# Kernel tuning notes

Measured on AMD Instinct MI355X. Metric: run time of the kernel, lower is better.

## Reference

```python
import jax, jax.numpy as jnp
import numpy as np

N = 1026; DX = 4096; DG = 4096; H0 = 4096; H1 = 2048; H2 = 1024
OUTS = 512; NL = 10; JH = 2048; E = 32832; K = 128; ALPHA = 0.05
INS = DX + DG  # 8192, edgeconv1 / joint_gemb input width

def _w(k, fan_in, shape):
    s = 1.0 / np.sqrt(fan_in)
    return jax.random.uniform(k, shape, minval=-s, maxval=s, dtype=jnp.float32)

def setup_inputs() -> dict:
    key = jax.random.key(0)
    ks = jax.random.split(key, 32)
    return dict(
        x=jax.random.normal(ks[0], (N, DX), jnp.float32),
        gx=jax.random.normal(ks[1], (N, DG), jnp.float32),
        edge_index=jax.random.randint(ks[2], (2, E), 0, N, dtype=jnp.int32),
        jw1=_w(ks[3], INS, (INS, JH)), jb1=_w(ks[4], INS, (JH,)),
        jw2=_w(ks[5], JH, (JH, N)), jb2=_w(ks[6], JH, (N,)),
        ec1_w=_w(ks[7], INS, (INS, H0)), ec1_b=_w(ks[8], INS, (H0,)),
        dr_w=_w(ks[9], H0, (H0, H2)), dr_b=_w(ks[10], H0, (H2,)),
        g1_w=_w(ks[11], H0, (H0, H1)), g1_b=_w(ks[12], H0, (H1,)),
        g2_w=_w(ks[13], H1, (H1, H2)), g2_b=_w(ks[14], H1, (H2,)),
        ec2_w=_w(ks[15], H2 + H1 + H0, (H2 + H1 + H0, H2)), ec2_b=_w(ks[16], H2 + H1 + H0, (H2,)),
        ec3_w=_w(ks[17], H2, (H2, OUTS)), ec3_b=_w(ks[18], H2, (OUTS,)),
        out_w=_w(ks[19], OUTS, (OUTS, NL)), out_b=_w(ks[20], OUTS, (NL,)),
    )

def _gdc(A):
    # GDC: self_loop_weight=1, sym norm in, exact PPR (alpha), topk(k, dim=0) sparsify, col norm out
    n = A.shape[0]
    eye = jnp.eye(n, dtype=A.dtype)
    A = A + eye  # self loops, weight 1
    deg = A.sum(axis=1)
    dinv = jax.lax.rsqrt(jnp.where(deg > 0, deg, 1.0))
    T = dinv[:, None] * A * dinv[None, :]          # D^-1/2 (A+I) D^-1/2
    S = ALPHA * jnp.linalg.inv(eye - (1.0 - ALPHA) * T)  # exact PPR diffusion
    vals, idx = jax.lax.top_k(S.T, K)              # top-K per column (dim=0)
    St = jnp.zeros((n, n), S.dtype).at[jnp.arange(n)[:, None], idx].set(vals)
    S = St.T
    csum = S.sum(axis=0)
    return S / jnp.where(csum == 0, 1.0, csum)[None, :]  # col normalization out

def _gcn(h_in, W, b, row, col, n):
    # PyG GCNConv: add self loops, sym-normalized aggregation, then bias
    h = h_in @ W
    deg = jax.ops.segment_sum(jnp.ones(row.shape[0], h.dtype), col, num_segments=n) + 1.0
    dinv = jax.lax.rsqrt(deg)
    agg = jax.ops.segment_sum(h[row] * (dinv[row] * dinv[col])[:, None], col, num_segments=n)
    return agg + h * (dinv * dinv)[:, None] + b

def _forward(x, gx, edge_index, jw1, jb1, jw2, jb2, ec1_w, ec1_b, dr_w, dr_b,
             g1_w, g1_b, g2_w, g2_b, ec2_w, ec2_b, ec3_w, ec3_b, out_w, out_b):
    row, col = edge_index[0], edge_index[1]
    xg = jnp.concatenate([x, gx], axis=1)                    # [N, INS]
    zz = jax.nn.relu(jax.nn.relu(xg @ jw1 + jb1) @ jw2 + jb2)  # joint_gemb -> [N, N] adjacency
    zz = _gdc(zz)
    xn = zz @ x                                              # nconv: dense neighbor aggregation
    z = jax.nn.relu(jnp.concatenate([xn, gx], axis=1) @ ec1_w + ec1_b)  # [N, H0]
    z0 = z @ dr_w + dr_b                                     # [N, H2]
    z1 = jax.nn.relu(_gcn(z + gx, g1_w, g1_b, row, col, N))  # [N, H1]
    z2 = jax.nn.relu(_gcn(z1, g2_w, g2_b, row, col, N))      # [N, H2]
    zc = jax.nn.relu(jnp.concatenate([z, z1, z2], axis=1) @ ec2_w + ec2_b)
    zf = jax.nn.relu((zc + z0) @ ec3_w + ec3_b)
    return zf @ out_w + out_b                                # [N, NL]

def reference(x, gx, edge_index, jw1, jb1, jw2, jb2, ec1_w, ec1_b, dr_w, dr_b,
              g1_w, g1_b, g2_w, g2_b, ec2_w, ec2_b, ec3_w, ec3_b, out_w, out_b):
    return _forward(x, gx, edge_index, jw1, jb1, jw2, jb2, ec1_w, ec1_b, dr_w, dr_b,
                    g1_w, g1_b, g2_w, g2_b, ec2_w, ec2_b, ec3_w, ec3_b, out_w, out_b)
```

## Files before the change

### kernel.cpp

```cpp
#include <hip/hip_runtime.h>
#include <stdint.h>

static constexpr int N_   = 1026;
static constexpr int DX_  = 4096;
static constexpr int DG_  = 4096;
static constexpr int H0_  = 4096;
static constexpr int H1_  = 2048;
static constexpr int H2_  = 1024;
static constexpr int OUTS_= 512;
static constexpr int NL_  = 10;
static constexpr int JH_  = 2048;
static constexpr int E_   = 32832;
static constexpr int K_   = 128;
static constexpr int INS_ = DX_ + DG_;
static constexpr int CAT2_= H0_ + H1_ + H2_;

static constexpr int MP_   = 1152;
static constexpr int KP1_  = 1056;

typedef _Float16 f16;
typedef __attribute__((ext_vector_type(8))) _Float16 f16x8;
typedef __attribute__((ext_vector_type(4))) _Float16 f16x4;
typedef __attribute__((ext_vector_type(4))) float    f32x4;

#define AS1C(p) ((const __attribute__((address_space(1))) unsigned int*)(p))
#define AS3(p)  ((__attribute__((address_space(3))) unsigned int*)(p))

__device__ __forceinline__ void gload16(const f16* g, f16* s) {
    __builtin_amdgcn_global_load_lds(AS1C(g), AS3(s), 16, 0, 0);
}

template<bool RELU, bool DUAL>
__global__ __launch_bounds__(512, DUAL ? 4 : 8)
void gemm_f16x2(int M, int Nc, int Kt, int chunkSteps,
                const f16* __restrict__ Ah, const f16* __restrict__ Al, int lda,
                const f16* __restrict__ Bh, const f16* __restrict__ Bl, int ldb,
                const float* __restrict__ bias, float alpha,
                const float* __restrict__ D, int ldd, float dscale,
                float* __restrict__ C, int ldc,
                f16* __restrict__ oAh, f16* __restrict__ oAl, int ldoa,
                f16* __restrict__ oBh, f16* __restrict__ oBl, int ldob,
                float* __restrict__ P, int Mp, int Ncp)
{
    __shared__ __align__(16) f16 sm[2][DUAL ? 4 : 2][4096];
    const int tid  = threadIdx.x;
    const int lane = tid & 63, w = tid >> 6;
    const int wr = w >> 1, wc = w & 1;
    const int bm = blockIdx.y * 128, bn = blockIdx.x * 128;
    const int z  = blockIdx.z;

    const int totalSteps = Kt >> 5;
    const int sBeg = z * chunkSteps;
    int nst = totalSteps - sBeg; if (nst > chunkSteps) nst = chunkSteps;

    const int srow  = w * 16 + (tid & 15);
    const int skoff = ((tid >> 4) & 3) * 8;
    const size_t arow = (size_t)(bm + srow) * lda + skoff;
    const size_t brow = (size_t)(bn + srow) * ldb + skoff;
    const int wslot = w * 512;
    const int fr = (lane >> 4) * 128 + (lane & 15) * 8;
    const int iaBase = wr * 1024 + fr;
    const int ibBase = wc * 2048 + fr;
    constexpr int PB = DUAL ? 8192 : 4096;

    f32x4 acc[2][4] = {};

    auto stage = [&](int buf, size_t ka) {
        f16* s0 = (f16*)&sm[buf][0][0];
        gload16(Ah + arow + ka, s0 + wslot);
        if constexpr (DUAL) gload16(Al + arow + ka, s0 + 4096 + wslot);
        gload16(Bh + brow + ka, s0 + PB + wslot);
        if constexpr (DUAL) gload16(Bl + brow + ka, s0 + PB + 4096 + wslot);
    };

    if (nst > 0) {
        const size_t kb = (size_t)sBeg * 32;
        stage(0, kb);
        for (int s = 0; s < nst; ++s) {
            if (s + 1 < nst) {
                stage((s + 1) & 1, kb + (size_t)(s + 1) * 32);
                if constexpr (DUAL)
                    asm volatile("s_waitcnt vmcnt(4)\n\ts_barrier" ::: "memory");
                else
                    asm volatile("s_waitcnt vmcnt(2)\n\ts_barrier" ::: "memory");
            } else {
                asm volatile("s_waitcnt vmcnt(0)\n\ts_barrier" ::: "memory");
            }
            const int b = s & 1;
            f16x8 ah[2], al[2], bh4[4], bl4[4];
            #pragma unroll
            for (int i = 0; i < 2; ++i) {
                ah[i] = *(const f16x8*)&sm[b][0][iaBase + i * 512];
                if constexpr (DUAL) al[i] = *(const f16x8*)&sm[b][1][iaBase + i * 512];
            }
            #pragma unroll
            for (int j = 0; j < 4; ++j) {
                bh4[j] = *(const f16x8*)&sm[b][DUAL ? 2 : 1][ibBase + j * 512];
                if constexpr (DUAL) bl4[j] = *(const f16x8*)&sm[b][3][ibBase + j * 512];
            }
            #pragma unroll
            for (int i = 0; i < 2; ++i)
                #pragma unroll
                for (int j = 0; j < 4; ++j) {
                    acc[i][j] = __builtin_amdgcn_mfma_f32_16x16x32_f16(ah[i], bh4[j], acc[i][j], 0, 0, 0);
                    if constexpr (DUAL) {
                        acc[i][j] = __builtin_amdgcn_mfma_f32_16x16x32_f16(ah[i], bl4[j], acc[i][j], 0, 0, 0);
                        acc[i][j] = __builtin_amdgcn_mfma_f32_16x16x32_f16(al[i], bh4[j], acc[i][j], 0, 0, 0);
                    }
                }
            if (s + 1 < nst) asm volatile("s_barrier" ::: "memory");
        }
    }

    const int er = (lane >> 4) * 4;
    const int ec = lane & 15;
    const int m00 = bm + wr * 32, n00 = bn + wc * 64;

    if (P) {
        float* Pz = P + (size_t)z * Mp * Ncp;
        #pragma unroll
        for (int mi = 0; mi < 2; ++mi)
            #pragma unroll
            for (int nj = 0; nj < 4; ++nj) {
                const int gc = n00 + nj * 16 + ec;
                const int gr = m00 + mi * 16 + er;
                float* p = Pz + (size_t)gr * Ncp + gc;
                f32x4 a = acc[mi][nj];
                #pragma unroll
                for (int r = 0; r < 4; ++r) p[(size_t)r * Ncp] = a[r];
            }
        return;
    }

    #pragma unroll
    for (int mi = 0; mi < 2; ++mi) {
        #pragma unroll
        for (int nj = 0; nj < 4; ++nj) {
            const int gcol = n00 + nj * 16 + ec;
            if (gcol >= Nc) continue;
            const float bv = bias ? bias[gcol] : 0.f;
            f32x4 a = acc[mi][nj];
            #pragma unroll
            for (int r = 0; r < 4; ++r) {
                const int grow = m00 + mi * 16 + er + r;
                if (grow >= M) continue;
                float val = alpha * a[r];
                if (D) val = fmaf(dscale, D[(size_t)grow * ldd + gcol], val);
                val += bv;
                if (RELU) val = fmaxf(val, 0.f);
                if (C) C[(size_t)grow * ldc + gcol] = val;
                if (oAh) {
                    f16 h = (f16)val, l = (f16)(val - (float)h);
                    oAh[(size_t)grow * ldoa + gcol] = h;
                    oAl[(size_t)grow * ldoa + gcol] = l;
                }
                if (oBh) {
                    f16 h = (f16)val, l = (f16)(val - (float)h);
                    oBh[(size_t)gcol * ldob + grow] = h;
                    oBl[(size_t)gcol * ldob + grow] = l;
                }
            }
        }
    }
}

template<bool RELU>
__global__ __launch_bounds__(256)
void combine_k(int M, int Nc, int nz, int Mp, int Ncp,
               const float* __restrict__ P,
               const float* __restrict__ bias, float alpha,
               const float* __restrict__ D, int ldd, float dscale,
               float* __restrict__ C, int ldc,
               f16* __restrict__ oAh, f16* __restrict__ oAl, int ldoa,
               f16* __restrict__ oBh, f16* __restrict__ oBl, int ldob)
{
    unsigned idx = blockIdx.x * 256 + threadIdx.x;
    if (idx >= (unsigned)(M * Nc)) return;
    int row = idx / (unsigned)Nc, col = idx - row * Nc;
    const float* p = P + (size_t)row * Ncp + col;
    float s = 0.f;
    for (int zz = 0; zz < nz; ++zz) s += p[(size_t)zz * Mp * Ncp];
    float val = alpha * s;
    if (D) val = fmaf(dscale, D[(size_t)row * ldd + col], val);
    if (bias) val += bias[col];
    if (RELU) val = fmaxf(val, 0.f);
    if (C) C[(size_t)row * ldc + col] = val;
    if (oAh) {
        f16 h = (f16)val, l = (f16)(val - (float)h);
        oAh[(size_t)row * ldoa + col] = h;
        oAl[(size_t)row * ldoa + col] = l;
    }
    if (oBh) {
        f16 h = (f16)val, l = (f16)(val - (float)h);
        oBh[(size_t)col * ldob + row] = h;
        oBl[(size_t)col * ldob + row] = l;
    }
}

__global__ __launch_bounds__(512, 4)
void pchain_k(int roleBase, int split, int chunkSteps,
              const f16* __restrict__ uAh, const f16* __restrict__ uAl,
              const f16* __restrict__ sAh, const f16* __restrict__ sAl,
              const f16* __restrict__ Bh, const f16* __restrict__ Bl,
              float* __restrict__ Pp)
{
    __shared__ __align__(16) f16 sm[2][4][4096];
    const int tid  = threadIdx.x;
    const int lane = tid & 63, w = tid >> 6;
    const int wr = w >> 1, wc = w & 1;
    const int bm = blockIdx.y * 128, bn = blockIdx.x * 128;
    const int z = blockIdx.z;
    const int role = roleBase + z / split;
    const int sub  = z % split;
    const f16* Ah = (role == 0) ? uAh : sAh;
    const f16* Al = (role == 0) ? uAl : sAl;

    const int sBeg = sub * chunkSteps;
    int nst = KP1_ / 32 - sBeg; if (nst > chunkSteps) nst = chunkSteps;

    const int srow  = w * 16 + (tid & 15);
    const int skoff = ((tid >> 4) & 3) * 8;
    const size_t arow = (size_t)(bm + srow) * KP1_ + skoff;
    const size_t brow = (size_t)(bn + srow) * KP1_ + skoff;
    const int wslot = w * 512;
    const int fr = (lane >> 4) * 128 + (lane & 15) * 8;
    const int iaBase = wr * 1024 + fr;
    const int ibBase = wc * 2048 + fr;

    f32x4 acc[2][4] = {};

    auto stage = [&](int buf, size_t ka) {
        f16* s0 = (f16*)&sm[buf][0][0];
        gload16(Ah + arow + ka, s0 + wslot);
        gload16(Al + arow + ka, s0 + 4096 + wslot);
        gload16(Bh + brow + ka, s0 + 8192 + wslot);
        gload16(Bl + brow + ka, s0 + 12288 + wslot);
    };

    const size_t kb = (size_t)sBeg * 32;
    stage(0, kb);
    for (int s = 0; s < nst; ++s) {
        if (s + 1 < nst) {
            stage((s + 1) & 1, kb + (size_t)(s + 1) * 32);
            asm volatile("s_waitcnt vmcnt(4)\n\ts_barrier" ::: "memory");
        } else {
            asm volatile("s_waitcnt vmcnt(0)\n\ts_barrier" ::: "memory");
        }
        const int b = s & 1;
        f16x8 ah[2], al[2], bh4[4], bl4[4];
        #pragma unroll
        for (int i = 0; i < 2; ++i) {
            ah[i]  = *(const f16x8*)&sm[b][0][iaBase + i * 512];
            al[i]  = *(const f16x8*)&sm[b][1][iaBase + i * 512];
        }
        #pragma unroll
        for (int j = 0; j < 4; ++j) {
            bh4[j] = *(const f16x8*)&sm[b][2][ibBase + j * 512];
            bl4[j] = *(const f16x8*)&sm[b][3][ibBase + j * 512];
        }
        #pragma unroll
        for (int i = 0; i < 2; ++i)
            #pragma unroll
            for (int j = 0; j < 4; ++j) {
                acc[i][j] = __builtin_amdgcn_mfma_f32_16x16x32_f16(ah[i], bh4[j], acc[i][j], 0, 0, 0);
                acc[i][j] = __builtin_amdgcn_mfma_f32_16x16x32_f16(ah[i], bl4[j], acc[i][j], 0, 0, 0);
                acc[i][j] = __builtin_amdgcn_mfma_f32_16x16x32_f16(al[i], bh4[j], acc[i][j], 0, 0, 0);
            }
        if (s + 1 < nst) asm volatile("s_barrier" ::: "memory");
    }

    float* Pz = Pp + (size_t)z * (1152 * 1152);
    const int er = (lane >> 4) * 4;
    const int ec = lane & 15;
    const int m00 = bm + wr * 32, n00 = bn + wc * 64;
    #pragma unroll
    for (int mi = 0; mi < 2; ++mi)
        #pragma unroll
        for (int nj = 0; nj < 4; ++nj) {
            const int gc = n00 + nj * 16 + ec;
            const int gr = m00 + mi * 16 + er;
            float* p = Pz + (size_t)gr * 1152 + gc;
            f32x4 a = acc[mi][nj];
            #pragma unroll
            for (int r = 0; r < 4; ++r) p[(size_t)r * 1152] = a[r];
        }
}

__global__ __launch_bounds__(256)
void pchain_combine_k(int nz, int hasUpd, int hasSq, const float* __restrict__ Pp,
                      const float* __restrict__ PfIn, float* __restrict__ PfOut,
                      f16* __restrict__ oPh, f16* __restrict__ oPl,
// ... 100 lines not shown
}

__global__ void conv_A_k(const float* __restrict__ src, int R, int C, int lds,
                         f16* __restrict__ dh, f16* __restrict__ dl, int ldd,
                         int Rp, int Cp)
{
    size_t i4 = ((size_t)blockIdx.x * 256 + threadIdx.x) * 4;
    if (i4 >= (size_t)Rp * Cp) return;
    int r = (int)(i4 / Cp), c = (int)(i4 % Cp);
    float v[4] = {0.f, 0.f, 0.f, 0.f};
    if (r < R) {
        if (((lds & 3) == 0) && c + 3 < C) {
            float4 f = *(const float4*)&src[(size_t)r * lds + c];
            v[0] = f.x; v[1] = f.y; v[2] = f.z; v[3] = f.w;
        } else {
            #pragma unroll
            for (int q = 0; q < 4; ++q) v[q] = (c + q < C) ? src[(size_t)r * lds + c + q] : 0.f;
        }
    }
    f16x4 h, l;
    #pragma unroll
    for (int q = 0; q < 4; ++q) { h[q] = (f16)v[q]; l[q] = (f16)(v[q] - (float)h[q]); }
    *(f16x4*)&dh[(size_t)r * ldd + c] = h;
    *(f16x4*)&dl[(size_t)r * ldd + c] = l;
}

__global__ __launch_bounds__(256)
void conv_Bt_k(const float* __restrict__ src, int K, int N,
               f16* __restrict__ dh, f16* __restrict__ dl, int ldk,
               int Kp, int Np)
{
    __shared__ float t[32][65];
    const int bk = blockIdx.x * 32, bn = blockIdx.y * 64;
    const int tid = threadIdx.x;
    {
        const int kk = tid >> 4;
        const int nn = (tid & 15) * 4;
        #pragma unroll
        for (int p = 0; p < 2; ++p) {
            int k = bk + kk + p * 16;
            float v[4] = {0.f, 0.f, 0.f, 0.f};
            if (k < K) {
                int n = bn + nn;
                if (((N & 3) == 0) && n + 3 < N) {
                    float4 f = *(const float4*)&src[(size_t)k * N + n];
                    v[0] = f.x; v[1] = f.y; v[2] = f.z; v[3] = f.w;
                } else {
// ... 1 lines not shown
                    for (int q = 0; q < 4; ++q) v[q] = (n + q < N) ? src[(size_t)k * N + n + q] : 0.f;
                }
            }
            #pragma unroll
            for (int q = 0; q < 4; ++q) t[kk + p * 16][nn + q] = v[q];
        }
    }
    __syncthreads();
    {
        const int nn0 = tid >> 3;
        const int k4  = (tid & 7) * 4;
        #pragma unroll
        for (int p = 0; p < 2; ++p) {
            int n = bn + nn0 + p * 32;
            int k = bk + k4;
            if (n < Np && k < Kp) {
                f16x4 h, l;
                #pragma unroll
                for (int q = 0; q < 4; ++q) {
                    float vv = t[k4 + q][nn0 + p * 32];
                    h[q] = (f16)vv; l[q] = (f16)(vv - (float)h[q]);
                }
                *(f16x4*)&dh[(size_t)n * ldk + k] = h;
                *(f16x4*)&dl[(size_t)n * ldk + k] = l;
            }
        }
    }
}

__global__ void cat2_conv_k(const float* __restrict__ a, const float* __restrict__ b,
                            f16* __restrict__ dh, f16* __restrict__ dl)
{
    size_t i4 = ((size_t)blockIdx.x * 256 + threadIdx.x) * 4;
    if (i4 >= (size_t)MP_ * 8192) return;
    int r = (int)(i4 / 8192), c = (int)(i4 % 8192);
    float v[4] = {0.f, 0.f, 0.f, 0.f};
    if (r < N_) {
        const float* s = (c < 4096) ? &a[(size_t)r * 4096 + c] : &b[(size_t)r * 4096 + (c - 4096)];
        float4 f = *(const float4*)s;
        v[0] = f.x; v[1] = f.y; v[2] = f.z; v[3] = f.w;
    }
    f16x4 h, l;
    #pragma unroll
    for (int q = 0; q < 4; ++q) { h[q] = (f16)v[q]; l[q] = (f16)(v[q] - (float)h[q]); }
    *(f16x4*)&dh[i4] = h;
    *(f16x4*)&dl[i4] = l;
}

__global__ void zgx_conv_k(const f16* __restrict__ zh, const f16* __restrict__ zl,
                           const float* __restrict__ gx,
                           f16* __restrict__ dh, f16* __restrict__ dl)
{
    size_t i4 = ((size_t)blockIdx.x * 256 + threadIdx.x) * 4;
    if (i4 >= (size_t)MP_ * 4096) return;
    int r = (int)(i4 / 4096), c = (int)(i4 % 4096);
    f16x4 h = {}, l = {};
    if (r < N_) {
        f16x4 zh4 = *(const f16x4*)&zh[(size_t)r * CAT2_ + c];
        f16x4 zl4 = *(const f16x4*)&zl[(size_t)r * CAT2_ + c];
        float4 g4 = *(const float4*)&gx[(size_t)r * 4096 + c];
        float gv[4] = {g4.x, g4.y, g4.z, g4.w};
        #pragma unroll
        for (int q = 0; q < 4; ++q) {
            float v = (float)zh4[q] + (float)zl4[q] + gv[q];
            h[q] = (f16)v; l[q] = (f16)(v - (float)h[q]);
        }
    }
    *(f16x4*)&dh[i4] = h;
    *(f16x4*)&dl[i4] = l;
}

__global__ void zc_conv_k(const float* __restrict__ zc, const float* __restrict__ z0,
                          f16* __restrict__ dh, f16* __restrict__ dl)
{
    size_t i4 = ((size_t)blockIdx.x * 256 + threadIdx.x) * 4;
    if (i4 >= (size_t)MP_ * 1024) return;
    int r = (int)(i4 / 1024), c = (int)(i4 % 1024);
    f16x4 h = {}, l = {};
    if (r < N_) {
        float4 a4 = *(const float4*)&zc[(size_t)r * 1024 + c];
        float4 b4 = *(const float4*)&z0[(size_t)r * 1024 + c];
        float av[4] = {a4.x, a4.y, a4.z, a4.w};
        float bv[4] = {b4.x, b4.y, b4.z, b4.w};
        #pragma unroll
        for (int q = 0; q < 4; ++q) {
            float v = av[q] + bv[q];
            h[q] = (f16)v; l[q] = (f16)(v - (float)h[q]);
        }
    }
    *(f16x4*)&dh[i4] = h;
    *(f16x4*)&dl[i4] = l;
}

template<int NPARTS, bool RELU>
__global__ __launch_bounds__(256)
void gemm_k(int M, int Nc, int Kt,
            const float* __restrict__ A0, int w0,
            const float* __restrict__ A1, int w1,
            const float* __restrict__ A2, int w2,
            const float* __restrict__ B, int ldb,
            const float* __restrict__ bias,
            float alpha, const float* __restrict__ D, float dscale,
            float* __restrict__ C, int ldc)
{
    __shared__ __align__(16) float As[16][68];
    __shared__ __align__(16) float Bs[16][68];
    const int tid = threadIdx.x;
    const int tx = tid & 15, ty = tid >> 4;
    const int bm = blockIdx.y * 64, bn = blockIdx.x * 64;
    const int w01 = w0 + w1;
    float acc[4][4] = {};

    for (int kt = 0; kt < Kt; kt += 16) {
        #pragma unroll
// ... 152 lines not shown
    __shared__ float deg[N_];
    int t = threadIdx.x;
    for (int i = t; i < N_; i += 1024) deg[i] = 1.f;
    __syncthreads();
    for (int e = t; e < E_; e += 1024) atomicAdd(&deg[ei[E_ + e]], 1.f);
    __syncthreads();
    for (int i = t; i < N_; i += 1024) dinv2[i] = 1.f / sqrtf(deg[i]);
}
__global__ void edge_diag_G_k(const int* __restrict__ ei, const float* __restrict__ dinv,
                              float* __restrict__ G) {
    int e = blockIdx.x * 256 + threadIdx.x;
    if (e < E_) {
        int r = ei[e], c = ei[E_ + e];
        atomicAdd(&G[(size_t)c * N_ + r], dinv[r] * dinv[c]);
    } else {
        int i = e - E_;
        if (i < N_) atomicAdd(&G[(size_t)i * N_ + i], dinv[i] * dinv[i]);
    }
}

struct HL { f16* h; f16* l; };
static const HL HL0 = {nullptr, nullptr};

static inline void g16(hipStream_t st, bool relu, bool dual, int M, int Nc, int Kt, int split,
                       HL A, int lda, HL B, int ldb,
                       const float* bias, float alpha,
                       const float* D, int ldd, float dscale,
                       float* C, int ldc,
                       HL oA, int ldoa, HL oB, int ldob, float* P)
{
    const int gx = (Nc + 127) / 128, gy = (M + 127) / 128;
    const int totalSteps = Kt >> 5;
    const int chunk = (totalSteps + split - 1) / split;
    const int Mp = gy * 128, Ncp = gx * 128;
    dim3 grid(gx, gy, split), blk(512);
    float* Pp = (split > 1) ? P : nullptr;
#define CALL_G16(RL, DU) gemm_f16x2<RL, DU><<<grid, blk, 0, st>>>(M, Nc, Kt, chunk, \
        A.h, A.l, lda, B.h, B.l, ldb, bias, alpha, D, ldd, dscale, C, ldc, \
        oA.h, oA.l, ldoa, oB.h, oB.l, ldob, Pp, Mp, Ncp)
    if (relu) { if (dual) CALL_G16(true, true); else CALL_G16(true, false); }
    else      { if (dual) CALL_G16(false, true); else CALL_G16(false, false); }
#undef CALL_G16
    if (split > 1) {
        unsigned tot = (unsigned)(M * Nc);
        dim3 cg((tot + 255) / 256);
        if (relu)
            combine_k<true><<<cg, 256, 0, st>>>(M, Nc, split, Mp, Ncp, P, bias, alpha,
                D, ldd, dscale, C, ldc, oA.h, oA.l, ldoa, oB.h, oB.l, ldob);
        else
            combine_k<false><<<cg, 256, 0, st>>>(M, Nc, split, Mp, Ncp, P, bias, alpha,
                D, ldd, dscale, C, ldc, oA.h, oA.l, ldoa, oB.h, oB.l, ldob);
    }
}

static inline void convA(hipStream_t st, const float* src, int R, int C, int lds,
                         HL d, int ldd, int Rp, int Cp)
{
    size_t total4 = (size_t)Rp * Cp / 4;
    conv_A_k<<<(int)((total4 + 255) / 256), 256, 0, st>>>(src, R, C, lds, d.h, d.l, ldd, Rp, Cp);
}
static inline void convBt(hipStream_t st, const float* src, int K, int N,
                          HL d, int ldk, int Kp, int Np)
{
    dim3 grid((Kp + 31) / 32, (Np + 63) / 64), blk(256);
// ... 58 lines not shown
static_assert(u_hg2Bt + 2 * hg2Bt_e <= UNION_F16, "phase3 alias");

static constexpr size_t o_catA2 = 0;
static constexpr size_t o_SA    = o_catA2 + 2 * catA2_e;
static constexpr size_t o_GA    = o_SA + 2 * SA_e;
static constexpr size_t o_xBt   = o_GA + 2 * GA_e;
static constexpr size_t o_zgxA  = o_xBt + 2 * xBt_e;
static constexpr size_t o_cat3  = o_zgxA + 2 * zgxA_e;
static constexpr size_t o_zcA   = o_cat3 + 2 * cat3_e;
static constexpr size_t OUT_F16 = o_zcA + 2 * zcA_e;

static constexpr size_t NN_     = (size_t)N_ * N_;
static constexpr size_t F16_TOTAL = UNION_F16 + OUT_F16;
static constexpr size_t f_zz = 0, f_Mm = NN_, f_X0 = 2 * NN_, f_X1 = 3 * NN_,
                        f_S = 4 * NN_, f_G = 5 * NN_, f_z0 = 6 * NN_,
                        f_zc = f_z0 + (size_t)N_ * 1024,
                        f_zf = f_zc + (size_t)N_ * 1024,
                        f_dinv = f_zf + (size_t)N_ * 512,
                        f_dinv2 = f_dinv + 1028,
                        F32_TOTAL = f_dinv2 + 1028;
static constexpr size_t P_e = (size_t)2 * MP_ * 4096;
static constexpr size_t FAST_WS_BYTES = F16_TOTAL * 2 + (F32_TOTAL + P_e) * 4;
static_assert((size_t)6 * 1152 * 1152 <= P_e, "pchain partial fit");

static void run_fast(void* const* d_in, float* out, void* d_ws, hipStream_t st)
{
    const float* x    = (const float*)d_in[0];
    const float* gx   = (const float*)d_in[1];
    const int*   ei   = (const int*)d_in[2];
    const float* jw1  = (const float*)d_in[3];
    const float* jb1  = (const float*)d_in[4];
    const float* jw2  = (const float*)d_in[5];
    const float* jb2  = (const float*)d_in[6];
    const float* ec1w = (const float*)d_in[7];
    const float* ec1b = (const float*)d_in[8];
    const float* drw  = (const float*)d_in[9];
    const float* drb  = (const float*)d_in[10];
    const float* g1w  = (const float*)d_in[11];
    const float* g1b  = (const float*)d_in[12];
    const float* g2w  = (const float*)d_in[13];
    const float* g2b  = (const float*)d_in[14];
    const float* ec2w = (const float*)d_in[15];
    const float* ec2b = (const float*)d_in[16];
    const float* ec3w = (const float*)d_in[17];
    const float* ec3b = (const float*)d_in[18];
    const float* outw = (const float*)d_in[19];
// ... 8 lines not shown
       jw2Bt = mk(u_jw2Bt, jw2Bt_e), h1A = mk(u_h1A, h1A_e);
    HL pA[2]  = {mk(u_nb0, nb_e), mk(u_nb1, nb_e)};
    HL aA[2]  = {mk(u_nb2, nb_e), mk(u_nb3, nb_e)};
    HL aBt[2] = {mk(u_nb4, nb_e), mk(u_nb5, nb_e)};
    HL ec1Bt = mk(0, ec1Bt_e);
    HL drBt = mk(u_drBt, drBt_e), g1Bt = mk(u_g1Bt, g1Bt_e), g2Bt = mk(u_g2Bt, g2Bt_e),
       ec2Bt = mk(u_ec2Bt, ec2Bt_e), ec3Bt = mk(u_ec3Bt, ec3Bt_e),
       hg1Bt = mk(u_hg1Bt, hg1Bt_e), hg2Bt = mk(u_hg2Bt, hg2Bt_e);
    HL catA2 = mk(UNION_F16 + o_catA2, catA2_e), SA = mk(UNION_F16 + o_SA, SA_e),
       GA = mk(UNION_F16 + o_GA, GA_e), xBt = mk(UNION_F16 + o_xBt, xBt_e),
       zgxA = mk(UNION_F16 + o_zgxA, zgxA_e), cat3 = mk(UNION_F16 + o_cat3, cat3_e),
       zcA = mk(UNION_F16 + o_zcA, zcA_e);
    float *zz = f32b + f_zz, *XT = f32b + f_Mm, *Pf[2] = {f32b + f_X0, f32b + f_X1},
          *S = f32b + f_S, *G = f32b + f_G, *z0 = f32b + f_z0, *zc = f32b + f_zc,
          *zf = f32b + f_zf, *dinv = f32b + f_dinv, *dinv2 = f32b + f_dinv2;

    hipMemsetAsync(fb + u_nb0, 0, (UNION_F16 - u_nb0) * sizeof(f16), st);

    {
        size_t t4 = (size_t)MP_ * 8192 / 4;
        cat2_conv_k<<<(int)((t4 + 255) / 256), 256, 0, st>>>(x, gx, catA1.h, catA1.l);
    }
    convBt(st, jw1, 8192, 2048, jw1Bt, 8192, 8192, 2048);
    g16(st, true, true, 1026, 2048, 8192, 4, catA1, 8192, jw1Bt, 8192, jb1, 1.f,
        nullptr, 0, 0.f, nullptr, 0, h1A, 2048, HL0, 0, P);
    convBt(st, jw2, 2048, 1026, jw2Bt, 2048, 2048, MP_);
    g16(st, true, true, 1026, 1026, 2048, 7, h1A, 2048, jw2Bt, 2048, jb2, 1.f,
        nullptr, 0, 0.f, zz, 1026, HL0, 0, HL0, 0, P);
    row_dinv_k<<<N_, 256, 0, st>>>(zz, dinv);
    build_A_k<<<(int)((NN_ + 255) / 256), 256, 0, st>>>(zz, dinv,
        aA[0].h, aA[0].l, aBt[0].h, aBt[0].l, Pf[0], pA[0].h, pA[0].l);
    {
        const int PS = 3, PCH = 11;
        dim3 cg((unsigned)((NN_ + 255) / 256));
        pchain_k<<<dim3(9, 9, PS), 512, 0, st>>>(1, PS, PCH,
            nullptr, nullptr, aA[0].h, aA[0].l, aBt[0].h, aBt[0].l, P);
        pchain_combine_k<<<cg, 256, 0, st>>>(PS, 0, 1, P,
            nullptr, nullptr, nullptr, nullptr, nullptr,
            aA[1].h, aA[1].l, aBt[1].h, aBt[1].l);
        int ac = 1, pc = 0;
        for (int k = 2; k <= 8; ++k) {
            pchain_k<<<dim3(9, 9, 2 * PS), 512, 0, st>>>(0, PS, PCH,
                pA[pc].h, pA[pc].l, aA[ac].h, aA[ac].l, aBt[ac].h, aBt[ac].l, P);
            pchain_combine_k<<<cg, 256, 0, st>>>(PS, 1, 1, P,
                Pf[pc], Pf[1 - pc], pA[1 - pc].h, pA[1 - pc].l, nullptr,
                aA[1 - ac].h, aA[1 - ac].l, aBt[1 - ac].h, aBt[1 - ac].l);
            pc ^= 1; ac ^= 1;
        }
        pchain_k<<<dim3(9, 9, PS), 512, 0, st>>>(0, PS, PCH,
            pA[pc].h, pA[pc].l, nullptr, nullptr, aBt[ac].h, aBt[ac].l, P);
        pchain_combine_k<<<cg, 256, 0, st>>>(PS, 1, 0, P,
            Pf[pc], Pf[1 - pc], nullptr, nullptr, XT,
            nullptr, nullptr, nullptr, nullptr);
    }
    hipMemsetAsync(S, 0, NN_ * sizeof(float), st);
    topk_sort_k<<<N_, 256, 0, st>>>(XT, S);
    convA(st, S, N_, N_, N_, SA, KP1_, MP_, KP1_);
    convBt(st, x, 1026, 4096, xBt, KP1_, KP1_, 4096);
    g16(st, false, true, 1026, 4096, KP1_, 2, SA, KP1_, xBt, KP1_, nullptr, 1.f,
        nullptr, 0, 0.f, nullptr, 0, HL{catA2.h, catA2.l}, 8192, HL0, 0, P);
    convA(st, gx, N_, 4096, 4096, HL{catA2.h + 4096, catA2.l + 4096}, 8192, MP_, 4096);
    convBt(st, ec1w, 8192, 4096, ec1Bt, 8192, 8192, 4096);
    g16(st, true, false, 1026, 4096, 8192, 2, catA2, 8192, ec1Bt, 8192, ec1b, 1.f,
        nullptr, 0, 0.f, nullptr, 0, HL{cat3.h, cat3.l}, 7168, HL0, 0, P);
    deg_dinv_k<<<1, 1024, 0, st>>>(ei, dinv2);
    hipMemsetAsync(G, 0, NN_ * sizeof(float), st);
    edge_diag_G_k<<<(E_ + N_ + 255) / 256, 256, 0, st>>>(ei, dinv2, G);
    convA(st, G, N_, N_, N_, GA, KP1_, MP_, KP1_);
    convBt(st, drw, 4096, 1024, drBt, 4096, 4096, 1024);
    g16(st, false, false, 1026, 1024, 4096, 8, HL{cat3.h, cat3.l}, 7168, drBt, 4096, drb, 1.f,
        nullptr, 0, 0.f, z0, 1024, HL0, 0, HL0, 0, P);
    {
        size_t t4 = (size_t)MP_ * 4096 / 4;
        zgx_conv_k<<<(int)((t4 + 255) / 256), 256, 0, st>>>(cat3.h, cat3.l, gx, zgxA.h, zgxA.l);
    }
    convBt(st, g1w, 4096, 2048, g1Bt, 4096, 4096, 2048);
    hipMemsetAsync(fb + u_hg1Bt, 0, (2 * hg1Bt_e + 2 * hg2Bt_e) * sizeof(f16), st);
    g16(st, false, false, 2048, 1026, 4096, 4, g1Bt, 4096, zgxA, 4096, nullptr, 1.f,
        nullptr, 0, 0.f, nullptr, 0, hg1Bt, KP1_, HL0, 0, P);
    g16(st, true, false, 1026, 2048, KP1_, 4, GA, KP1_, hg1Bt, KP1_, g1b, 1.f,
        nullptr, 0, 0.f, nullptr, 0, HL{cat3.h + 4096, cat3.l + 4096}, 7168, HL0, 0, P);
    convBt(st, g2w, 2048, 1024, g2Bt, 2048, 2048, 1024);
    g16(st, false, false, 1024, 1026, 2048, 8, g2Bt, 2048, HL{cat3.h + 4096, cat3.l + 4096}, 7168,
        nullptr, 1.f, nullptr, 0, 0.f, nullptr, 0, hg2Bt, KP1_, HL0, 0, P);
    g16(st, true, false, 1026, 1024, KP1_, 8, GA, KP1_, hg2Bt, KP1_, g2b, 1.f,
        nullptr, 0, 0.f, nullptr, 0, HL{cat3.h + 6144, cat3.l + 6144}, 7168, HL0, 0, P);
    convBt(st, ec2w, 7168, 1024, ec2Bt, 7168, 7168, 1024);
    g16(st, true, false, 1026, 1024, 7168, 8, cat3, 7168, ec2Bt, 7168, ec2b, 1.f,
        nullptr, 0, 0.f, zc, 1024, HL0, 0, HL0, 0, P);
    {
        size_t t4 = (size_t)MP_ * 1024 / 4;
        zc_conv_k<<<(int)((t4 + 255) / 256), 256, 0, st>>>(zc, z0, zcA.h, zcA.l);
    }
    convBt(st, ec3w, 1024, 512, ec3Bt, 1024, 1024, 512);
    g16(st, true, false, 1026, 512, 1024, 8, zcA, 1024, ec3Bt, 1024, ec3b, 1.f,
        nullptr, 0, 0.f, zf, 512, HL0, 0, HL0, 0, P);
    launch_gemm_f32(st, false, 1, N_, NL_, OUTS_, zf, OUTS_, nullptr, 0, nullptr, 0,
                    outw, NL_, outb, 1.f, nullptr, 0.f, out, NL_);
}

static void run_ref(void* const* d_in, float* out, void* d_ws, hipStream_t stream)
{
    const float* x    = (const float*)d_in[0];
    const float* gx   = (const float*)d_in[1];
    const int*   ei   = (const int*)d_in[2];
    const float* jw1  = (const float*)d_in[3];
    const float* jb1  = (const float*)d_in[4];
    const float* jw2  = (const float*)d_in[5];
    const float* jb2  = (const float*)d_in[6];
    const float* ec1w = (const float*)d_in[7];
    const float* ec1b = (const float*)d_in[8];
    const float* drw  = (const float*)d_in[9];
    const float* drb  = (const float*)d_in[10];
    const float* g1w  = (const float*)d_in[11];
    const float* g1b  = (const float*)d_in[12];
    const float* g2w  = (const float*)d_in[13];
    const float* g2b  = (const float*)d_in[14];
    const float* ec2w = (const float*)d_in[15];
    const float* ec2b = (const float*)d_in[16];
// ... 84 lines not shown
```

Measured before the change: 1.618 ms.

## Add wide 128x256 GEMM tiles, XCD-aware tile swizzle, drop unused low halves, shorten PPR chain

New measurement: 1.478 ms. 1.09x faster.

```diff
diff --git a/kernel.cpp b/kernel.cpp
--- a/kernel.cpp
+++ b/kernel.cpp
@@ -30,8 +30,17 @@
     __builtin_amdgcn_global_load_lds(AS1C(g), AS3(s), 16, 0, 0);
 }
 
-template<bool RELU, bool DUAL>
-__global__ __launch_bounds__(512, DUAL ? 4 : 8)
+__device__ __forceinline__ void swz_tile(int gx, int gy, int& bx, int& by) {
+    int nwg = gx * gy;
+    int hid = blockIdx.x + gx * blockIdx.y;
+    int xcd = hid & 7, seq = hid >> 3;
+    int q = nwg >> 3, r = nwg & 7;
+    int lin = (xcd < r ? xcd * (q + 1) : r * (q + 1) + (xcd - r) * q) + seq;
+    bx = lin / gy;  by = lin - bx * gy;
+}
+
+template<bool RELU, bool DUAL, bool WIDE>
+__global__ __launch_bounds__(512, (DUAL || WIDE) ? 4 : 8)
 void gemm_f16x2(int M, int Nc, int Kt, int chunkSteps,
                 const f16* __restrict__ Ah, const f16* __restrict__ Al, int lda,
                 const f16* __restrict__ Bh, const f16* __restrict__ Bl, int ldb,
@@ -42,11 +51,18 @@
                 f16* __restrict__ oBh, f16* __restrict__ oBl, int ldob,
                 float* __restrict__ P, int Mp, int Ncp)
 {
-    __shared__ __align__(16) f16 sm[2][DUAL ? 4 : 2][4096];
+    static_assert(!(DUAL && WIDE), "dual+wide unsupported");
+    constexpr int BUFE = DUAL ? 16384 : (WIDE ? 12288 : 8192);
+    constexpr int BN   = WIDE ? 256 : 128;
+    constexpr int NJ   = WIDE ? 8 : 4;
+    constexpr int BOFF = DUAL ? 8192 : 4096;
+    __shared__ __align__(16) f16 sm[2 * BUFE];
+
     const int tid  = threadIdx.x;
     const int lane = tid & 63, w = tid >> 6;
     const int wr = w >> 1, wc = w & 1;
-    const int bm = blockIdx.y * 128, bn = blockIdx.x * 128;
+    int bx, by; swz_tile(gridDim.x, gridDim.y, bx, by);
+    const int bm = by * 128, bn = bx * BN;
     const int z  = blockIdx.z;
 
     const int totalSteps = Kt >> 5;
@@ -55,22 +71,23 @@
 
     const int srow  = w * 16 + (tid & 15);
     const int skoff = ((tid >> 4) & 3) * 8;
-    const size_t arow = (size_t)(bm + srow) * lda + skoff;
-    const size_t brow = (size_t)(bn + srow) * ldb + skoff;
+    const size_t arow  = (size_t)(bm + srow) * lda + skoff;
+    const size_t brow  = (size_t)(bn + srow) * ldb + skoff;
+    const size_t brow2 = WIDE ? ((size_t)(bn + 128 + srow) * ldb + skoff) : 0;
     const int wslot = w * 512;
     const int fr = (lane >> 4) * 128 + (lane & 15) * 8;
     const int iaBase = wr * 1024 + fr;
-    const int ibBase = wc * 2048 + fr;
-    constexpr int PB = DUAL ? 8192 : 4096;
-
-    f32x4 acc[2][4] = {};
+    const int ibBase = BOFF + wc * (WIDE ? 4096 : 2048) + fr;
+
+    f32x4 acc[2][NJ] = {};
 
     auto stage = [&](int buf, size_t ka) {
-        f16* s0 = (f16*)&sm[buf][0][0];
+        f16* s0 = sm + buf * BUFE;
         gload16(Ah + arow + ka, s0 + wslot);
         if constexpr (DUAL) gload16(Al + arow + ka, s0 + 4096 + wslot);
-        gload16(Bh + brow + ka, s0 + PB + wslot);
-        if constexpr (DUAL) gload16(Bl + brow + ka, s0 + PB + 4096 + wslot);
+        gload16(Bh + brow + ka, s0 + BOFF + wslot);
+        if constexpr (DUAL) gload16(Bl + brow + ka, s0 + BOFF + 4096 + wslot);
+        if constexpr (WIDE) gload16(Bh + brow2 + ka, s0 + BOFF + 4096 + wslot);
     };
 
     if (nst > 0) {
@@ -81,27 +98,29 @@
                 stage((s + 1) & 1, kb + (size_t)(s + 1) * 32);
                 if constexpr (DUAL)
                     asm volatile("s_waitcnt vmcnt(4)\n\ts_barrier" ::: "memory");
+                else if constexpr (WIDE)
+                    asm volatile("s_waitcnt vmcnt(3)\n\ts_barrier" ::: "memory");
                 else
                     asm volatile("s_waitcnt vmcnt(2)\n\ts_barrier" ::: "memory");
             } else {
                 asm volatile("s_waitcnt vmcnt(0)\n\ts_barrier" ::: "memory");
             }
-            const int b = s & 1;
-            f16x8 ah[2], al[2], bh4[4], bl4[4];
+            const f16* sb = sm + (s & 1) * BUFE;
+            f16x8 ah[2], al[2], bh4[NJ], bl4[NJ];
             #pragma unroll
             for (int i = 0; i < 2; ++i) {
-                ah[i] = *(const f16x8*)&sm[b][0][iaBase + i * 512];
-                if constexpr (DUAL) al[i] = *(const f16x8*)&sm[b][1][iaBase + i * 512];
+                ah[i] = *(const f16x8*)&sb[iaBase + i * 512];
+                if constexpr (DUAL) al[i] = *(const f16x8*)&sb[4096 + iaBase + i * 512];
             }
             #pragma unroll
-            for (int j = 0; j < 4; ++j) {
-                bh4[j] = *(const f16x8*)&sm[b][DUAL ? 2 : 1][ibBase + j * 512];
-                if constexpr (DUAL) bl4[j] = *(const f16x8*)&sm[b][3][ibBase + j * 512];
+            for (int j = 0; j < NJ; ++j) {
+                bh4[j] = *(const f16x8*)&sb[ibBase + j * 512];
+                if constexpr (DUAL) bl4[j] = *(const f16x8*)&sb[4096 + ibBase + j * 512];
             }
             #pragma unroll
             for (int i = 0; i < 2; ++i)
                 #pragma unroll
-                for (int j = 0; j < 4; ++j) {
+                for (int j = 0; j < NJ; ++j) {
                     acc[i][j] = __builtin_amdgcn_mfma_f32_16x16x32_f16(ah[i], bh4[j], acc[i][j], 0, 0, 0);
                     if constexpr (DUAL) {
                         acc[i][j] = __builtin_amdgcn_mfma_f32_16x16x32_f16(ah[i], bl4[j], acc[i][j], 0, 0, 0);
@@ -114,14 +133,14 @@
 
     const int er = (lane >> 4) * 4;
     const int ec = lane & 15;
-    const int m00 = bm + wr * 32, n00 = bn + wc * 64;
+    const int m00 = bm + wr * 32, n00 = bn + wc * (WIDE ? 128 : 64);
 
     if (P) {
         float* Pz = P + (size_t)z * Mp * Ncp;
         #pragma unroll
         for (int mi = 0; mi < 2; ++mi)
             #pragma unroll
-            for (int nj = 0; nj < 4; ++nj) {
+            for (int nj = 0; nj < NJ; ++nj) {
                 const int gc = n00 + nj * 16 + ec;
                 const int gr = m00 + mi * 16 + er;
                 float* p = Pz + (size_t)gr * Ncp + gc;
@@ -135,7 +154,7 @@
     #pragma unroll
     for (int mi = 0; mi < 2; ++mi) {
         #pragma unroll
-        for (int nj = 0; nj < 4; ++nj) {
+        for (int nj = 0; nj < NJ; ++nj) {
             const int gcol = n00 + nj * 16 + ec;
             if (gcol >= Nc) continue;
             const float bv = bias ? bias[gcol] : 0.f;
@@ -150,14 +169,14 @@
                 if (RELU) val = fmaxf(val, 0.f);
                 if (C) C[(size_t)grow * ldc + gcol] = val;
                 if (oAh) {
-                    f16 h = (f16)val, l = (f16)(val - (float)h);
+                    f16 h = (f16)val;
                     oAh[(size_t)grow * ldoa + gcol] = h;
-                    oAl[(size_t)grow * ldoa + gcol] = l;
+                    if (oAl) oAl[(size_t)grow * ldoa + gcol] = (f16)(val - (float)h);
                 }
                 if (oBh) {
-                    f16 h = (f16)val, l = (f16)(val - (float)h);
+                    f16 h = (f16)val;
                     oBh[(size_t)gcol * ldob + grow] = h;
-                    oBl[(size_t)gcol * ldob + grow] = l;
+                    if (oBl) oBl[(size_t)gcol * ldob + grow] = (f16)(val - (float)h);
                 }
             }
         }
@@ -186,14 +205,14 @@
     if (RELU) val = fmaxf(val, 0.f);
     if (C) C[(size_t)row * ldc + col] = val;
     if (oAh) {
-        f16 h = (f16)val, l = (f16)(val - (float)h);
+        f16 h = (f16)val;
         oAh[(size_t)row * ldoa + col] = h;
-        oAl[(size_t)row * ldoa + col] = l;
+        if (oAl) oAl[(size_t)row * ldoa + col] = (f16)(val - (float)h);
     }
     if (oBh) {
-        f16 h = (f16)val, l = (f16)(val - (float)h);
+        f16 h = (f16)val;
         oBh[(size_t)col * ldob + row] = h;
-        oBl[(size_t)col * ldob + row] = l;
+        if (oBl) oBl[(size_t)col * ldob + row] = (f16)(val - (float)h);
     }
 }
 
@@ -208,7 +227,8 @@
     const int tid  = threadIdx.x;
     const int lane = tid & 63, w = tid >> 6;
     const int wr = w >> 1, wc = w & 1;
-    const int bm = blockIdx.y * 128, bn = blockIdx.x * 128;
+    int bx, by; swz_tile(gridDim.x, gridDim.y, bx, by);
+    const int bm = by * 128, bn = bx * 128;
     const int z = blockIdx.z;
     const int role = roleBase + z / split;
     const int sub  = z % split;
@@ -237,36 +257,38 @@
         gload16(Bl + brow + ka, s0 + 12288 + wslot);
     };
 
-    const size_t kb = (size_t)sBeg * 32;
-    stage(0, kb);
-    for (int s = 0; s < nst; ++s) {
-        if (s + 1 < nst) {
-            stage((s + 1) & 1, kb + (size_t)(s + 1) * 32);
-            asm volatile("s_waitcnt vmcnt(4)\n\ts_barrier" ::: "memory");
-        } else {
-            asm volatile("s_waitcnt vmcnt(0)\n\ts_barrier" ::: "memory");
-        }
-        const int b = s & 1;
-        f16x8 ah[2], al[2], bh4[4], bl4[4];
-        #pragma unroll
-        for (int i = 0; i < 2; ++i) {
-            ah[i]  = *(const f16x8*)&sm[b][0][iaBase + i * 512];
-            al[i]  = *(const f16x8*)&sm[b][1][iaBase + i * 512];
-        }
-        #pragma unroll
-        for (int j = 0; j < 4; ++j) {
-            bh4[j] = *(const f16x8*)&sm[b][2][ibBase + j * 512];
-            bl4[j] = *(const f16x8*)&sm[b][3][ibBase + j * 512];
-        }
-        #pragma unroll
-        for (int i = 0; i < 2; ++i)
+    if (nst > 0) {
+        const size_t kb = (size_t)sBeg * 32;
+        stage(0, kb);
+        for (int s = 0; s < nst; ++s) {
+            if (s + 1 < nst) {
+                stage((s + 1) & 1, kb + (size_t)(s + 1) * 32);
+                asm volatile("s_waitcnt vmcnt(4)\n\ts_barrier" ::: "memory");
+            } else {
+                asm volatile("s_waitcnt vmcnt(0)\n\ts_barrier" ::: "memory");
+            }
+            const int b = s & 1;
+            f16x8 ah[2], al[2], bh4[4], bl4[4];
+            #pragma unroll
+            for (int i = 0; i < 2; ++i) {
+                ah[i]  = *(const f16x8*)&sm[b][0][iaBase + i * 512];
+                al[i]  = *(const f16x8*)&sm[b][1][iaBase + i * 512];
+            }
             #pragma unroll
             for (int j = 0; j < 4; ++j) {
-                acc[i][j] = __builtin_amdgcn_mfma_f32_16x16x32_f16(ah[i], bh4[j], acc[i][j], 0, 0, 0);
-                acc[i][j] = __builtin_amdgcn_mfma_f32_16x16x32_f16(ah[i], bl4[j], acc[i][j], 0, 0, 0);
-                acc[i][j] = __builtin_amdgcn_mfma_f32_16x16x32_f16(al[i], bh4[j], acc[i][j], 0, 0, 0);
+                bh4[j] = *(const f16x8*)&sm[b][2][ibBase + j * 512];
+                bl4[j] = *(const f16x8*)&sm[b][3][ibBase + j * 512];
             }
-        if (s + 1 < nst) asm volatile("s_barrier" ::: "memory");
+            #pragma unroll
+            for (int i = 0; i < 2; ++i)
+                #pragma unroll
+                for (int j = 0; j < 4; ++j) {
+                    acc[i][j] = __builtin_amdgcn_mfma_f32_16x16x32_f16(ah[i], bh4[j], acc[i][j], 0, 0, 0);
+                    acc[i][j] = __builtin_amdgcn_mfma_f32_16x16x32_f16(ah[i], bl4[j], acc[i][j], 0, 0, 0);
+                    acc[i][j] = __builtin_amdgcn_mfma_f32_16x16x32_f16(al[i], bh4[j], acc[i][j], 0, 0, 0);
+                }
+            if (s + 1 < nst) asm volatile("s_barrier" ::: "memory");
+        }
     }
 
     float* Pz = Pp + (size_t)z * (1152 * 1152);
@@ -413,7 +435,7 @@
     #pragma unroll
     for (int q = 0; q < 4; ++q) { h[q] = (f16)v[q]; l[q] = (f16)(v[q] - (float)h[q]); }
     *(f16x4*)&dh[(size_t)r * ldd + c] = h;
-    *(f16x4*)&dl[(size_t)r * ldd + c] = l;
+    if (dl) *(f16x4*)&dl[(size_t)r * ldd + c] = l;
 }
 
 __global__ __launch_bounds__(256)
@@ -461,7 +483,7 @@
                     h[q] = (f16)vv; l[q] = (f16)(vv - (float)h[q]);
                 }
                 *(f16x4*)&dh[(size_t)n * ldk + k] = h;
-                *(f16x4*)&dl[(size_t)n * ldk + k] = l;
+                if (dl) *(f16x4*)&dl[(size_t)n * ldk + k] = l;
             }
         }
     }
@@ -486,49 +508,39 @@
     *(f16x4*)&dl[i4] = l;
 }
 
-__global__ void zgx_conv_k(const f16* __restrict__ zh, const f16* __restrict__ zl,
-                           const float* __restrict__ gx,
-                           f16* __restrict__ dh, f16* __restrict__ dl)
+__global__ void zgx_conv_k(const f16* __restrict__ zh, const float* __restrict__ gx,
+                           f16* __restrict__ dh)
 {
     size_t i4 = ((size_t)blockIdx.x * 256 + threadIdx.x) * 4;
     if (i4 >= (size_t)MP_ * 4096) return;
     int r = (int)(i4 / 4096), c = (int)(i4 % 4096);
-    f16x4 h = {}, l = {};
+    f16x4 h = {};
     if (r < N_) {
         f16x4 zh4 = *(const f16x4*)&zh[(size_t)r * CAT2_ + c];
-        f16x4 zl4 = *(const f16x4*)&zl[(size_t)r * CAT2_ + c];
         float4 g4 = *(const float4*)&gx[(size_t)r * 4096 + c];
         float gv[4] = {g4.x, g4.y, g4.z, g4.w};
         #pragma unroll
-        for (int q = 0; q < 4; ++q) {
-            float v = (float)zh4[q] + (float)zl4[q] + gv[q];
-            h[q] = (f16)v; l[q] = (f16)(v - (float)h[q]);
-        }
+        for (int q = 0; q < 4; ++q) h[q] = (f16)((float)zh4[q] + gv[q]);
     }
     *(f16x4*)&dh[i4] = h;
-    *(f16x4*)&dl[i4] = l;
 }
 
 __global__ void zc_conv_k(const float* __restrict__ zc, const float* __restrict__ z0,
-                          f16* __restrict__ dh, f16* __restrict__ dl)
+                          f16* __restrict__ dh)
 {
     size_t i4 = ((size_t)blockIdx.x * 256 + threadIdx.x) * 4;
     if (i4 >= (size_t)MP_ * 1024) return;
     int r = (int)(i4 / 1024), c = (int)(i4 % 1024);
-    f16x4 h = {}, l = {};
+    f16x4 h = {};
     if (r < N_) {
         float4 a4 = *(const float4*)&zc[(size_t)r * 1024 + c];
         float4 b4 = *(const float4*)&z0[(size_t)r * 1024 + c];
         float av[4] = {a4.x, a4.y, a4.z, a4.w};
         float bv[4] = {b4.x, b4.y, b4.z, b4.w};
         #pragma unroll
-        for (int q = 0; q < 4; ++q) {
-            float v = av[q] + bv[q];
-            h[q] = (f16)v; l[q] = (f16)(v - (float)h[q]);
-        }
+        for (int q = 0; q < 4; ++q) h[q] = (f16)(av[q] + bv[q]);
     }
     *(f16x4*)&dh[i4] = h;
-    *(f16x4*)&dl[i4] = l;
 }
 
 template<int NPARTS, bool RELU>
@@ -727,24 +739,27 @@
 struct HL { f16* h; f16* l; };
 static const HL HL0 = {nullptr, nullptr};
 
-static inline void g16(hipStream_t st, bool relu, bool dual, int M, int Nc, int Kt, int split,
+static inline void g16(hipStream_t st, bool relu, bool dual, bool wide,
+                       int M, int Nc, int Kt, int split,
                        HL A, int lda, HL B, int ldb,
                        const float* bias, float alpha,
                        const float* D, int ldd, float dscale,
                        float* C, int ldc,
                        HL oA, int ldoa, HL oB, int ldob, float* P)
 {
-    const int gx = (Nc + 127) / 128, gy = (M + 127) / 128;
+    const int BN = wide ? 256 : 128;
+    const int gx = (Nc + BN - 1) / BN, gy = (M + 127) / 128;
     const int totalSteps = Kt >> 5;
     const int chunk = (totalSteps + split - 1) / split;
-    const int Mp = gy * 128, Ncp = gx * 128;
+    const int Mp = gy * 128, Ncp = gx * BN;
     dim3 grid(gx, gy, split), blk(512);
     float* Pp = (split > 1) ? P : nullptr;
-#define CALL_G16(RL, DU) gemm_f16x2<RL, DU><<<grid, blk, 0, st>>>(M, Nc, Kt, chunk, \
+#define CALL_G16(RL, DU, WI) gemm_f16x2<RL, DU, WI><<<grid, blk, 0, st>>>(M, Nc, Kt, chunk, \
         A.h, A.l, lda, B.h, B.l, ldb, bias, alpha, D, ldd, dscale, C, ldc, \
         oA.h, oA.l, ldoa, oB.h, oB.l, ldob, Pp, Mp, Ncp)
-    if (relu) { if (dual) CALL_G16(true, true); else CALL_G16(true, false); }
-    else      { if (dual) CALL_G16(false, true); else CALL_G16(false, false); }
+    if (dual)      { if (relu) CALL_G16(true, true, false);  else CALL_G16(false, true, false); }
+    else if (wide) { if (relu) CALL_G16(true, false, true);  else CALL_G16(false, false, true); }
+    else           { if (relu) CALL_G16(true, false, false); else CALL_G16(false, false, false); }
 #undef CALL_G16
     if (split > 1) {
         unsigned tot = (unsigned)(M * Nc);
@@ -849,6 +864,8 @@
 static constexpr size_t P_e = (size_t)2 * MP_ * 4096;
 static constexpr size_t FAST_WS_BYTES = F16_TOTAL * 2 + (F32_TOTAL + P_e) * 4;
 static_assert((size_t)6 * 1152 * 1152 <= P_e, "pchain partial fit");
+static_assert((size_t)8 * 1152 * 1024 <= P_e, "wide split8 fit");
+static_assert((size_t)4 * 1152 * 2048 <= P_e, "wide split4 fit");
 
 static void run_fast(void* const* d_in, float* out, void* d_ws, hipStream_t st)
 {
@@ -903,10 +920,10 @@
         cat2_conv_k<<<(int)((t4 + 255) / 256), 256, 0, st>>>(x, gx, catA1.h, catA1.l);
     }
     convBt(st, jw1, 8192, 2048, jw1Bt, 8192, 8192, 2048);
-    g16(st, true, true, 1026, 2048, 8192, 4, catA1, 8192, jw1Bt, 8192, jb1, 1.f,
+    g16(st, true, true, false, 1026, 2048, 8192, 4, catA1, 8192, jw1Bt, 8192, jb1, 1.f,
         nullptr, 0, 0.f, nullptr, 0, h1A, 2048, HL0, 0, P);
     convBt(st, jw2, 2048, 1026, jw2Bt, 2048, 2048, MP_);
-    g16(st, true, true, 1026, 1026, 2048, 7, h1A, 2048, jw2Bt, 2048, jb2, 1.f,
+    g16(st, true, true, false, 1026, 1026, 2048, 7, h1A, 2048, jw2Bt, 2048, jb2, 1.f,
         nullptr, 0, 0.f, zz, 1026, HL0, 0, HL0, 0, P);
     row_dinv_k<<<N_, 256, 0, st>>>(zz, dinv);
     build_A_k<<<(int)((NN_ + 255) / 256), 256, 0, st>>>(zz, dinv,
@@ -920,7 +937,7 @@
             nullptr, nullptr, nullptr, nullptr, nullptr,
             aA[1].h, aA[1].l, aBt[1].h, aBt[1].l);
         int ac = 1, pc = 0;
-        for (int k = 2; k <= 8; ++k) {
+        for (int k = 2; k <= 7; ++k) {
             pchain_k<<<dim3(9, 9, 2 * PS), 512, 0, st>>>(0, PS, PCH,
                 pA[pc].h, pA[pc].l, aA[ac].h, aA[ac].l, aBt[ac].h, aBt[ac].l, P);
             pchain_combine_k<<<cg, 256, 0, st>>>(PS, 1, 1, P,
@@ -938,44 +955,45 @@
     topk_sort_k<<<N_, 256, 0, st>>>(XT, S);
     convA(st, S, N_, N_, N_, SA, KP1_, MP_, KP1_);
     convBt(st, x, 1026, 4096, xBt, KP1_, KP1_, 4096);
-    g16(st, false, true, 1026, 4096, KP1_, 2, SA, KP1_, xBt, KP1_, nullptr, 1.f,
-        nullptr, 0, 0.f, nullptr, 0, HL{catA2.h, catA2.l}, 8192, HL0, 0, P);
-    convA(st, gx, N_, 4096, 4096, HL{catA2.h + 4096, catA2.l + 4096}, 8192, MP_, 4096);
-    convBt(st, ec1w, 8192, 4096, ec1Bt, 8192, 8192, 4096);
-    g16(st, true, false, 1026, 4096, 8192, 2, catA2, 8192, ec1Bt, 8192, ec1b, 1.f,
-        nullptr, 0, 0.f, nullptr, 0, HL{cat3.h, cat3.l}, 7168, HL0, 0, P);
+    g16(st, false, true, false, 1026, 4096, KP1_, 2, SA, KP1_, xBt, KP1_, nullptr, 1.f,
+        nullptr, 0, 0.f, nullptr, 0, HL{catA2.h, nullptr}, 8192, HL0, 0, P);
+    convA(st, gx, N_, 4096, 4096, HL{catA2.h + 4096, nullptr}, 8192, MP_, 4096);
+    convBt(st, ec1w, 8192, 4096, HL{ec1Bt.h, nullptr}, 8192, 8192, 4096);
+    g16(st, true, false, true, 1026, 4096, 8192, 2, catA2, 8192, ec1Bt, 8192, ec1b, 1.f,
+        nullptr, 0, 0.f, nullptr, 0, HL{cat3.h, nullptr}, 7168, HL0, 0, P);
     deg_dinv_k<<<1, 1024, 0, st>>>(ei, dinv2);
     hipMemsetAsync(G, 0, NN_ * sizeof(float), st);
     edge_diag_G_k<<<(E_ + N_ + 255) / 256, 256, 0, st>>>(ei, dinv2, G);
-    convA(st, G, N_, N_, N_, GA, KP1_, MP_, KP1_);
-    convBt(st, drw, 4096, 1024, drBt, 4096, 4096, 1024);
-    g16(st, false, false, 1026, 1024, 4096, 8, HL{cat3.h, cat3.l}, 7168, drBt, 4096, drb, 1.f,
-        nullptr, 0, 0.f, z0, 1024, HL0, 0, HL0, 0, P);
+    convA(st, G, N_, N_, N_, HL{GA.h, nullptr}, KP1_, MP_, KP1_);
+    convBt(st, drw, 4096, 1024, HL{drBt.h, nullptr}, 4096, 4096, 1024);
+    g16(st, false, false, true, 1026, 1024, 4096, 8, HL{cat3.h, nullptr}, 7168,
+        drBt, 4096, drb, 1.f, nullptr, 0, 0.f, z0, 1024, HL0, 0, HL0, 0, P);
     {
         size_t t4 = (size_t)MP_ * 4096 / 4;
-        zgx_conv_k<<<(int)((t4 + 255) / 256), 256, 0, st>>>(cat3.h, cat3.l, gx, zgxA.h, zgxA.l);
-    }
-    convBt(st, g1w, 4096, 2048, g1Bt, 4096, 4096, 2048);
+        zgx_conv_k<<<(int)((t4 + 255) / 256), 256, 0, st>>>(cat3.h, gx, zgxA.h);
+    }
+    convBt(st, g1w, 4096, 2048, HL{g1Bt.h, nullptr}, 4096, 4096, 2048);
     hipMemsetAsync(fb + u_hg1Bt, 0, (2 * hg1Bt_e + 2 * hg2Bt_e) * sizeof(f16), st);
-    g16(st, false, false, 2048, 1026, 4096, 4, g1Bt, 4096, zgxA, 4096, nullptr, 1.f,
-        nullptr, 0, 0.f, nullptr, 0, hg1Bt, KP1_, HL0, 0, P);
-    g16(st, true, false, 1026, 2048, KP1_, 4, GA, KP1_, hg1Bt, KP1_, g1b, 1.f,
-        nullptr, 0, 0.f, nullptr, 0, HL{cat3.h + 4096, cat3.l + 4096}, 7168, HL0, 0, P);
-    convBt(st, g2w, 2048, 1024, g2Bt, 2048, 2048, 1024);
-    g16(st, false, false, 1024, 1026, 2048, 8, g2Bt, 2048, HL{cat3.h + 4096, cat3.l + 4096}, 7168,
-        nullptr, 1.f, nullptr, 0, 0.f, nullptr, 0, hg2Bt, KP1_, HL0, 0, P);
-    g16(st, true, false, 1026, 1024, KP1_, 8, GA, KP1_, hg2Bt, KP1_, g2b, 1.f,
-        nullptr, 0, 0.f, nullptr, 0, HL{cat3.h + 6144, cat3.l + 6144}, 7168, HL0, 0, P);
-    convBt(st, ec2w, 7168, 1024, ec2Bt, 7168, 7168, 1024);
-    g16(st, true, false, 1026, 1024, 7168, 8, cat3, 7168, ec2Bt, 7168, ec2b, 1.f,
-        nullptr, 0, 0.f, zc, 1024, HL0, 0, HL0, 0, P);
+    g16(st, false, false, false, 2048, 1026, 4096, 4, g1Bt, 4096, zgxA, 4096, nullptr, 1.f,
+        nullptr, 0, 0.f, nullptr, 0, HL{hg1Bt.h, nullptr}, KP1_, HL0, 0, P);
+    g16(st, true, false, true, 1026, 2048, KP1_, 4, GA, KP1_, hg1Bt, KP1_, g1b, 1.f,
+        nullptr, 0, 0.f, nullptr, 0, HL{cat3.h + 4096, nullptr}, 7168, HL0, 0, P);
+    convBt(st, g2w, 2048, 1024, HL{g2Bt.h, nullptr}, 2048, 2048, 1024);
+    g16(st, false, false, false, 1024, 1026, 2048, 8, g2Bt, 2048,
+        HL{cat3.h + 4096, nullptr}, 7168, nullptr, 1.f, nullptr, 0, 0.f,
+        nullptr, 0, HL{hg2Bt.h, nullptr}, KP1_, HL0, 0, P);
+    g16(st, true, false, true, 1026, 1024, KP1_, 8, GA, KP1_, hg2Bt, KP1_, g2b, 1.f,
+        nullptr, 0, 0.f, nullptr, 0, HL{cat3.h + 6144, nullptr}, 7168, HL0, 0, P);
+    convBt(st, ec2w, 7168, 1024, HL{ec2Bt.h, nullptr}, 7168, 7168, 1024);
+    g16(st, true, false, true, 1026, 1024, 7168, 8, HL{cat3.h, nullptr}, 7168,
+        ec2Bt, 7168, ec2b, 1.f, nullptr, 0, 0.f, zc, 1024, HL0, 0, HL0, 0, P);
     {
         size_t t4 = (size_t)MP_ * 1024 / 4;
-        zc_conv_k<<<(int)((t4 + 255) / 256), 256, 0, st>>>(zc, z0, zcA.h, zcA.l);
-    }
-    convBt(st, ec3w, 1024, 512, ec3Bt, 1024, 1024, 512);
-    g16(st, true, false, 1026, 512, 1024, 8, zcA, 1024, ec3Bt, 1024, ec3b, 1.f,
-        nullptr, 0, 0.f, zf, 512, HL0, 0, HL0, 0, P);
+        zc_conv_k<<<(int)((t4 + 255) / 256), 256, 0, st>>>(zc, z0, zcA.h);
+    }
+    convBt(st, ec3w, 1024, 512, HL{ec3Bt.h, nullptr}, 1024, 1024, 512);
+    g16(st, true, false, false, 1026, 512, 1024, 8, HL{zcA.h, nullptr}, 1024,
+        ec3Bt, 1024, ec3b, 1.f, nullptr, 0, 0.f, zf, 512, HL0, 0, HL0, 0, P);
     launch_gemm_f32(st, false, 1, N_, NL_, OUTS_, zf, OUTS_, nullptr, 0, nullptr, 0,
                     outw, NL_, outb, 1.f, nullptr, 0.f, out, NL_);
 }
```
